# Performance work log

Hardware: AMD Instinct MI355X
Metric: run time of the kernel (lower is better)

## Reference

```python
import jax, jax.numpy as jnp
import numpy as np

H = 1024
W = 1024
N = 128
K1 = 21.7  # on-road exponential loss scale
K2 = 40.0  # off-road exponential loss scale


def setup_inputs() -> dict:
    key = jax.random.key(0)
    k1, k2 = jax.random.split(key)
    hd_map = (jax.random.uniform(k1, (H, W)) < 0.3).astype(jnp.float32)
    # integer pixel coordinates, kept away from the border so the 2x2
    # neighbor window is always in-bounds (matches typical usage)
    prediction = jax.random.randint(k2, (N, 2), 2, H - 2).astype(jnp.int32)
    return {"hd_map": hd_map, "prediction": prediction}


def reference(hd_map, prediction):
    Hm, Wm = hd_map.shape
    p = prediction.astype(jnp.float32)  # [N,2]

    # Separable squared distances from each point to every pixel.
    # NOTE: faithful to the original, nonzero()[:,0] (row) is compared with
    # point[0] and nonzero()[:,1] (col) with point[1].
    rows = jnp.arange(Hm, dtype=jnp.float32)
    cols = jnp.arange(Wm, dtype=jnp.float32)
    dr2 = (rows[None, :] - p[:, 0:1]) ** 2  # [N,H]
    dc2 = (cols[None, :] - p[:, 1:2]) ** 2  # [N,W]
    d2 = dr2[:, :, None] + dc2[:, None, :]  # [N,H,W]

    INF = jnp.float32(1e30)
    on_mask = hd_map != 0  # nonzero pixels of hd_map (non-drivable)
    # min squared distance to nearest nonzero pixel of hd_map
    d2_on = jnp.min(jnp.where(on_mask[None], d2, INF), axis=(1, 2))  # [N]
    # min squared distance to nearest nonzero pixel of (1 - hd_map)
    d2_off = jnp.min(jnp.where(on_mask[None], INF, d2), axis=(1, 2))  # [N]

    px = prediction[:, 0]
    py = prediction[:, 1]
    # is_outside_frame: point[0] vs shape[0], point[1] vs shape[1] (faithful)
    outside_frame = (px < 0) | (px > Hm) | (py < 0) | (py > Wm)

    # is_outside_road: 2x2 window im[py-1:py+1, px-1:px+1] contains a 1
    ir = jnp.stack([py - 1, py - 1, py, py], axis=-1)  # [N,4]
    ic = jnp.stack([px - 1, px, px - 1, px], axis=-1)  # [N,4]
    neigh = hd_map[ir, ic]  # [N,4]
    outside_road = jnp.any(neigh == 1.0, axis=-1)

    ln2 = jnp.log(jnp.float32(2.0))
    # off-road: exp(d * ln(2)/k2); on-road: exp(-d^2 / k1)
    loss_off = jnp.exp(jnp.sqrt(d2_off) * (ln2 / K2))
    loss_on = jnp.exp(-d2_on / K1)

    per_point = jnp.where(
        outside_frame,
        jnp.float32(0.0),
        jnp.where(outside_road, loss_off, loss_on),
    )
    return jnp.mean(per_point)
```

## Files before the change

kernel.cpp:

```cpp
#include <hip/hip_runtime.h>
#include <math.h>

#define HMAP 1024
#define WMAP 1024

__device__ __forceinline__ int clampi(int x, int hi) {
    return x < 0 ? 0 : (x > hi ? hi : x);
}

__global__ __launch_bounds__(64)
void roadloss_scan(const float* __restrict__ hd_map,
                   const int* __restrict__ pred,
                   int n,
                   float* __restrict__ out,
                   float* __restrict__ ws) {
    const int pt   = blockIdx.x;
    const int lane = threadIdx.x;
    const int px = pred[2 * pt];
    const int py = pred[2 * pt + 1];

    const int r0c = clampi(py - 1, HMAP - 1), r1c = clampi(py, HMAP - 1);
    const int c0c = clampi(px - 1, WMAP - 1), c1c = clampi(px, WMAP - 1);
    const float n00 = hd_map[r0c * WMAP + c0c];
    const float n01 = hd_map[r0c * WMAP + c1c];
    const float n10 = hd_map[r1c * WMAP + c0c];
    const float n11 = hd_map[r1c * WMAP + c1c];

    float best_on = 1e30f, best_off = 1e30f;

    const int R = 16;
#pragma unroll
    for (int ii = 0; ii < 18; ++ii) {
        int i = lane + ii * 64;
        if (i < 33 * 33) {
            int dr = i / 33 - R;
            int dc = i % 33 - R;
            int r = px + dr, c = py + dc;
            if ((unsigned)r < (unsigned)HMAP && (unsigned)c < (unsigned)WMAP) {
                float v  = hd_map[r * WMAP + c];
                float d2 = (float)(dr * dr + dc * dc);
                if (v != 0.0f) best_on  = fminf(best_on,  d2);
                else           best_off = fminf(best_off, d2);
            }
        }
    }
#pragma unroll
    for (int s = 1; s < 64; s <<= 1) {
        best_on  = fminf(best_on,  __shfl_xor(best_on,  s, 64));
        best_off = fminf(best_off, __shfl_xor(best_off, s, 64));
    }

    const float guard = (float)((R + 1) * (R + 1));
    if (!(best_on <= guard && best_off <= guard)) {
        for (int i = lane; i < HMAP * WMAP; i += 64) {
            int r = i >> 10, c = i & (WMAP - 1);
            int dri = r - px, dci = c - py;
            float d2 = (float)(dri * dri + dci * dci);
            float v = hd_map[i];
            if (v != 0.0f) best_on  = fminf(best_on,  d2);
            else           best_off = fminf(best_off, d2);
        }
#pragma unroll
        for (int s = 1; s < 64; s <<= 1) {
            best_on  = fminf(best_on,  __shfl_xor(best_on,  s, 64));
            best_off = fminf(best_off, __shfl_xor(best_off, s, 64));
        }
    }

    if (lane == 0) {
        bool outside_frame = (px < 0) | (px > HMAP) | (py < 0) | (py > WMAP);
        bool outside_road  = (n00 == 1.0f) | (n01 == 1.0f) |
                             (n10 == 1.0f) | (n11 == 1.0f);
        const float K1 = 21.7f, K2 = 40.0f;
        const float LN2 = 0.6931471805599453f;
        float loss = outside_frame
                         ? 0.0f
                         : (outside_road ? expf(sqrtf(best_off) * (LN2 / K2))
                                         : expf(-best_on / K1));
        atomicAdd(&ws[0], loss);
        __threadfence();
        unsigned old = atomicAdd((unsigned int*)(ws + 1), 1u);
        if (old == (unsigned)(n - 1)) {
            float total = atomicAdd(&ws[0], 0.0f);
            out[0] = total / (float)n;
        }
    }
}

extern "C" void kernel_launch(void* const* d_in, const int* in_sizes, int n_in,
                              void* d_out, int out_size, void* d_ws, size_t ws_size,
                              hipStream_t stream) {
    const float* hd_map = (const float*)d_in[0];
    const int*   pred   = (const int*)d_in[1];
    float* out = (float*)d_out;
    float* ws  = (float*)d_ws;
    int n = in_sizes[1] / 2;

    hipMemsetAsync(ws, 0, 2 * sizeof(float), stream);
    roadloss_scan<<<n, 64, 0, stream>>>(hd_map, pred, n, out, ws);
}
```

Baseline: 65.17 us.

## Use cooperative grid sync for final reduction and batch window loads

Replaces the memset plus atomic counter final reduction with a cooperative launch: each block writes its per-point loss to workspace, the grid synchronizes, and block 0 sums and averages. This removes the separate memset launch and the atomics. The 33x33 window loads are also hoisted into a register array with clamped addresses so all 18 loads issue before the min computation, and two accumulator pairs split the dependency chain. Cooperative launch adds grid-sync overhead and has its own launch cost.

```diff
diff --git a/kernel.cpp b/kernel.cpp
--- a/kernel.cpp
+++ b/kernel.cpp
@@ -1,5 +1,8 @@
 #include <hip/hip_runtime.h>
+#include <hip/hip_cooperative_groups.h>
 #include <math.h>
+
+namespace cg = cooperative_groups;
 
 #define HMAP 1024
 #define WMAP 1024
@@ -9,81 +12,105 @@
 }
 
 __global__ __launch_bounds__(64)
-void roadloss_scan(const float* __restrict__ hd_map,
+void roadloss_coop(const float* __restrict__ hd_map,
                    const int* __restrict__ pred,
                    int n,
                    float* __restrict__ out,
                    float* __restrict__ ws) {
     const int pt   = blockIdx.x;
     const int lane = threadIdx.x;
-    const int px = pred[2 * pt];
-    const int py = pred[2 * pt + 1];
 
-    const int r0c = clampi(py - 1, HMAP - 1), r1c = clampi(py, HMAP - 1);
-    const int c0c = clampi(px - 1, WMAP - 1), c1c = clampi(px, WMAP - 1);
-    const float n00 = hd_map[r0c * WMAP + c0c];
-    const float n01 = hd_map[r0c * WMAP + c1c];
-    const float n10 = hd_map[r1c * WMAP + c0c];
-    const float n11 = hd_map[r1c * WMAP + c1c];
+    if (pt < n) {
+        const int px = pred[2 * pt];
+        const int py = pred[2 * pt + 1];
 
-    float best_on = 1e30f, best_off = 1e30f;
+        const int r0c = clampi(py - 1, HMAP - 1), r1c = clampi(py, HMAP - 1);
+        const int c0c = clampi(px - 1, WMAP - 1), c1c = clampi(px, WMAP - 1);
+        const float n00 = hd_map[r0c * WMAP + c0c];
+        const float n01 = hd_map[r0c * WMAP + c1c];
+        const float n10 = hd_map[r1c * WMAP + c0c];
+        const float n11 = hd_map[r1c * WMAP + c1c];
 
-    const int R = 16;
+        const int R = 16;
+
+        float v[18];
 #pragma unroll
-    for (int ii = 0; ii < 18; ++ii) {
-        int i = lane + ii * 64;
-        if (i < 33 * 33) {
+        for (int ii = 0; ii < 18; ++ii) {
+            int i  = lane + ii * 64;
             int dr = i / 33 - R;
             int dc = i % 33 - R;
-            int r = px + dr, c = py + dc;
-            if ((unsigned)r < (unsigned)HMAP && (unsigned)c < (unsigned)WMAP) {
-                float v  = hd_map[r * WMAP + c];
-                float d2 = (float)(dr * dr + dc * dc);
-                if (v != 0.0f) best_on  = fminf(best_on,  d2);
-                else           best_off = fminf(best_off, d2);
+            int r  = clampi(px + dr, HMAP - 1);
+            int c  = clampi(py + dc, WMAP - 1);
+            v[ii]  = hd_map[r * WMAP + c];
+        }
+
+        float on0 = 1e30f, off0 = 1e30f, on1 = 1e30f, off1 = 1e30f;
+#pragma unroll
+        for (int ii = 0; ii < 18; ++ii) {
+            int i  = lane + ii * 64;
+            int dr = i / 33 - R;
+            int dc = i % 33 - R;
+            bool inb = (i < 33 * 33) &&
+                       ((unsigned)(px + dr) < (unsigned)HMAP) &&
+                       ((unsigned)(py + dc) < (unsigned)WMAP);
+            float d2 = (float)(dr * dr + dc * dc);
+            if (inb) {
+                if (ii & 1) {
+                    if (v[ii] != 0.0f) on1  = fminf(on1,  d2);
+                    else               off1 = fminf(off1, d2);
+                } else {
+                    if (v[ii] != 0.0f) on0  = fminf(on0,  d2);
+                    else               off0 = fminf(off0, d2);
+                }
             }
         }
-    }
-#pragma unroll
-    for (int s = 1; s < 64; s <<= 1) {
-        best_on  = fminf(best_on,  __shfl_xor(best_on,  s, 64));
-        best_off = fminf(best_off, __shfl_xor(best_off, s, 64));
-    }
+        float best_on  = fminf(on0,  on1);
+        float best_off = fminf(off0, off1);
 
-    const float guard = (float)((R + 1) * (R + 1));
-    if (!(best_on <= guard && best_off <= guard)) {
-        for (int i = lane; i < HMAP * WMAP; i += 64) {
-            int r = i >> 10, c = i & (WMAP - 1);
-            int dri = r - px, dci = c - py;
-            float d2 = (float)(dri * dri + dci * dci);
-            float v = hd_map[i];
-            if (v != 0.0f) best_on  = fminf(best_on,  d2);
-            else           best_off = fminf(best_off, d2);
-        }
 #pragma unroll
         for (int s = 1; s < 64; s <<= 1) {
             best_on  = fminf(best_on,  __shfl_xor(best_on,  s, 64));
             best_off = fminf(best_off, __shfl_xor(best_off, s, 64));
         }
-    }
 
-    if (lane == 0) {
-        bool outside_frame = (px < 0) | (px > HMAP) | (py < 0) | (py > WMAP);
-        bool outside_road  = (n00 == 1.0f) | (n01 == 1.0f) |
-                             (n10 == 1.0f) | (n11 == 1.0f);
-        const float K1 = 21.7f, K2 = 40.0f;
-        const float LN2 = 0.6931471805599453f;
-        float loss = outside_frame
+        const float guard = (float)((R + 1) * (R + 1));
+        if (!(best_on <= guard && best_off <= guard)) {
+            for (int i = lane; i < HMAP * WMAP; i += 64) {
+                int r = i >> 10, c = i & (WMAP - 1);
+                int dri = r - px, dci = c - py;
+                float d2 = (float)(dri * dri + dci * dci);
+                float m = hd_map[i];
+                if (m != 0.0f) best_on  = fminf(best_on,  d2);
+                else           best_off = fminf(best_off, d2);
+            }
+#pragma unroll
+            for (int s = 1; s < 64; s <<= 1) {
+                best_on  = fminf(best_on,  __shfl_xor(best_on,  s, 64));
+                best_off = fminf(best_off, __shfl_xor(best_off, s, 64));
+            }
+        }
+
+        if (lane == 0) {
+            bool outside_frame = (px < 0) | (px > HMAP) | (py < 0) | (py > WMAP);
+            bool outside_road  = (n00 == 1.0f) | (n01 == 1.0f) |
+                                 (n10 == 1.0f) | (n11 == 1.0f);
+            const float K1 = 21.7f, K2 = 40.0f;
+            const float LN2 = 0.6931471805599453f;
+            ws[pt] = outside_frame
                          ? 0.0f
                          : (outside_road ? expf(sqrtf(best_off) * (LN2 / K2))
                                          : expf(-best_on / K1));
-        atomicAdd(&ws[0], loss);
-        __threadfence();
-        unsigned old = atomicAdd((unsigned int*)(ws + 1), 1u);
-        if (old == (unsigned)(n - 1)) {
-            float total = atomicAdd(&ws[0], 0.0f);
-            out[0] = total / (float)n;
         }
+    }
+
+    cg::this_grid().sync();
+
+    if (blockIdx.x == 0) {
+        float s = 0.0f;
+        for (int i = lane; i < n; i += 64) s += ws[i];
+#pragma unroll
+        for (int d = 1; d < 64; d <<= 1) s += __shfl_xor(s, d, 64);
+        if (lane == 0) out[0] = s / (float)n;
     }
 }
 
@@ -96,6 +123,8 @@
     float* ws  = (float*)d_ws;
     int n = in_sizes[1] / 2;
 
-    hipMemsetAsync(ws, 0, 2 * sizeof(float), stream);
-    roadloss_scan<<<n, 64, 0, stream>>>(hd_map, pred, n, out, ws);
+    void* args[] = {(void*)&hd_map, (void*)&pred, (void*)&n,
+                    (void*)&out, (void*)&ws};
+    hipLaunchCooperativeKernel((const void*)roadloss_coop,
+                               dim3((unsigned)n), dim3(64), args, 0, stream);
 }
```

After: 86.14 us. 32.2% more time.
